# Kernel optimization log

Measured on AMD Instinct MI355X. Metric: run time of the kernel, lower is better.

Reference implementation:

```python
import math
import jax, jax.numpy as jnp
import numpy as np

B, S, D, H = 4, 2048, 1024, 16
DK = D // H
THETA = 10000.0


def _rope(xh, pos):
    # xh: [B, H, S, DK], pos: [S]
    half = jnp.arange(0, DK, 2, dtype=jnp.float32) / DK
    inv_freq = THETA ** (-half)                      # [DK/2]
    ang = pos.astype(jnp.float32)[:, None] * inv_freq  # [S, DK/2]
    cos, sin = jnp.cos(ang).astype(xh.dtype), jnp.sin(ang).astype(xh.dtype)
    x1, x2 = xh[..., 0::2], xh[..., 1::2]
    r1 = x1 * cos - x2 * sin
    r2 = x1 * sin + x2 * cos
    return jnp.stack([r1, r2], axis=-1).reshape(xh.shape)


def setup_inputs() -> dict:
    key = jax.random.key(0)
    kx, kq, kk, kv, ko = jax.random.split(key, 5)
    std = 0.02
    x = jax.random.normal(kx, (B, S, D), jnp.float32)
    wq = jax.random.normal(kq, (D, D), jnp.float32) * std
    wk = jax.random.normal(kk, (D, D), jnp.float32) * std
    wv = jax.random.normal(kv, (D, D), jnp.float32) * std
    wo = jax.random.normal(ko, (D, D), jnp.float32) * std
    token_positions = jnp.arange(S, dtype=jnp.int32)
    return {"x": x, "wq": wq, "wk": wk, "wv": wv, "wo": wo,
            "token_positions": token_positions}


def reference(x, wq, wk, wv, wo, token_positions):
    # bias-free linear projections: y = x @ W^T (torch Linear convention)
    q = x @ wq.T
    k = x @ wk.T
    v = x @ wv.T
    # split heads: [B, S, D] -> [B, H, S, DK]
    to_heads = lambda t: t.reshape(B, S, H, DK).transpose(0, 2, 1, 3)
    qh, kh, vh = to_heads(q), to_heads(k), to_heads(v)
    qh = _rope(qh, token_positions)
    kh = _rope(kh, token_positions)
    scores = jnp.einsum('bhqd,bhkd->bhqk', qh, kh) / math.sqrt(DK)
    causal = jnp.tril(jnp.ones((S, S), dtype=bool))
    scores = jnp.where(causal, scores, -jnp.inf)
    attn = jax.nn.softmax(scores, axis=-1)
    out = jnp.einsum('bhqk,bhkd->bhqd', attn, vh)       # [B, H, S, DK]
    out = out.transpose(0, 2, 1, 3).reshape(B, S, D)    # merge heads
    return out @ wo.T
```

## Files before the change

kernel.cpp:

```cpp
#include <hip/hip_runtime.h>

#define B_ 4
#define S_ 2048
#define D_ 1024
#define H_ 16
#define DK_ 64
#define M_ (B_*S_)
#define K_ D_
#define N_ D_
#define NSTEP 32

typedef unsigned short u16;
typedef unsigned int u32;
typedef __bf16 bf16x8 __attribute__((ext_vector_type(8)));
typedef float f32x4 __attribute__((ext_vector_type(4)));
typedef u32 u32x4v __attribute__((ext_vector_type(4)));

#define EXP2F(x) __builtin_amdgcn_exp2f(x)

__device__ __forceinline__ u16 f2bf(float f) {
    u32 u = __builtin_bit_cast(u32, f);
    u += 0x7fff + ((u >> 16) & 1);
    return (u16)(u >> 16);
}
__device__ __forceinline__ float bf2f(u16 h) {
    u32 u = ((u32)h) << 16;
    return __builtin_bit_cast(float, u);
}
__device__ __forceinline__ u32 pack_trunc(float a, float b) {
    return (__builtin_bit_cast(u32, a) >> 16) | (__builtin_bit_cast(u32, b) & 0xffff0000u);
}

#define GLDS16(g, l) __builtin_amdgcn_global_load_lds( \
    (__attribute__((address_space(1))) void*)(g),      \
    (__attribute__((address_space(3))) void*)(l), 16, 0, 0)

__global__ __launch_bounds__(256) void cvt_all(
    const float* __restrict__ x,
    const float* __restrict__ w0, const float* __restrict__ w1,
    const float* __restrict__ w2, const float* __restrict__ w3,
    u16* __restrict__ xb,
    u16* __restrict__ o0, u16* __restrict__ o1,
    u16* __restrict__ o2, u16* __restrict__ o3) {
    const size_t i = (size_t)blockIdx.x * 256 + threadIdx.x;
    const float* in;
    u16* out;
    size_t off;
    if (i < 2097152) {
        in = x; out = xb; off = i;
    } else {
        const size_t j = i - 2097152;
        const int wi = (int)(j >> 18);
        off = j & 262143;
        in  = (wi == 0) ? w0 : (wi == 1) ? w1 : (wi == 2) ? w2 : w3;
        out = (wi == 0) ? o0 : (wi == 1) ? o1 : (wi == 2) ? o2 : o3;
    }
    const float4 f = *(const float4*)(in + off * 4);
    u32 p0 = (u32)f2bf(f.x) | ((u32)f2bf(f.y) << 16);
    u32 p1 = (u32)f2bf(f.z) | ((u32)f2bf(f.w) << 16);
    *(uint2*)(out + off * 4) = make_uint2(p0, p1);
}

template <int MODE>
__device__ __forceinline__ void gemm_tile(const u16* __restrict__ A,
                                          const u16* __restrict__ Bm,
                                          void* __restrict__ Cv,
                                          int m0, int n0,
                                          u16* __restrict__ As,
                                          u16* __restrict__ Bs) {
    const int tid  = threadIdx.x;
    const int wave = tid >> 6, lane = tid & 63;
    const int wm = wave & 1, wn = wave >> 1;
    const int quad = lane >> 4, mcol = lane & 15;

    const int c0 = wave, c1 = wave + 4;
    const int r0 = c0 * 16 + (lane >> 2), r1 = c1 * 16 + (lane >> 2);
    const int kb = (((lane & 3) ^ ((lane >> 3) & 3)) * 8);
    const u16* ga0 = A  + (size_t)(m0 + r0) * K_ + kb;
    const u16* ga1 = A  + (size_t)(m0 + r1) * K_ + kb;
    const u16* gb0 = Bm + (size_t)(n0 + r0) * K_ + kb;
    const u16* gb1 = Bm + (size_t)(n0 + r1) * K_ + kb;
    const int lo0 = c0 * 512, lo1 = c1 * 512;
    const int rsw = ((mcol >> 1) & 3);

    f32x4 acc[4][4];
#pragma unroll
    for (int i = 0; i < 4; i++)
#pragma unroll
        for (int j = 0; j < 4; j++) acc[i][j] = f32x4{0.f, 0.f, 0.f, 0.f};

    GLDS16(ga0, As + lo0); GLDS16(ga1, As + lo1);
    GLDS16(gb0, Bs + lo0); GLDS16(gb1, Bs + lo1);
    ga0 += 32; ga1 += 32; gb0 += 32; gb1 += 32;

    int cur = 0;
    for (int t = 0; t < NSTEP; ++t) {
        asm volatile("s_waitcnt vmcnt(0)" ::: "memory");
        asm volatile("s_waitcnt lgkmcnt(0)" ::: "memory");
        __builtin_amdgcn_s_barrier();

        if (t + 1 < NSTEP) {
            u16* at = As + (cur ^ 1) * 4096;
            u16* bt = Bs + (cur ^ 1) * 4096;
            GLDS16(ga0, at + lo0); GLDS16(ga1, at + lo1);
            GLDS16(gb0, bt + lo0); GLDS16(gb1, bt + lo1);
            ga0 += 32; ga1 += 32; gb0 += 32; gb1 += 32;
        }

        const u16* Ab = As + cur * 4096;
        const u16* Bb = Bs + cur * 4096;
        bf16x8 af[4], bfr[4];
#pragma unroll
        for (int i = 0; i < 4; i++) {
            af[i]  = *(const bf16x8*)&Ab[(wm * 64 + i * 16 + mcol) * 32 + (quad ^ rsw) * 8];
            bfr[i] = *(const bf16x8*)&Bb[(wn * 64 + i * 16 + mcol) * 32 + (quad ^ rsw) * 8];
        }
        __builtin_amdgcn_s_setprio(1);
#pragma unroll
        for (int i = 0; i < 4; i++)
#pragma unroll
            for (int j = 0; j < 4; j++)
                acc[i][j] = __builtin_amdgcn_mfma_f32_16x16x32_bf16(
                    af[i], bfr[j], acc[i][j], 0, 0, 0);
        __builtin_amdgcn_s_setprio(0);

        cur ^= 1;
    }

#pragma unroll
    for (int i = 0; i < 4; i++) {
        const int row = m0 + wm * 64 + i * 16 + quad * 4;
#pragma unroll
        for (int j = 0; j < 4; j++) {
            const int col = n0 + wn * 64 + j * 16 + mcol;
            if constexpr (MODE == 2) {
                const int hh = col >> 6, dd = col & 63;
                const int bb = row >> 11, ss = row & 2047;
                const u32 lo = (u32)f2bf(acc[i][j][0]) | ((u32)f2bf(acc[i][j][1]) << 16);
                const u32 hi = (u32)f2bf(acc[i][j][2]) | ((u32)f2bf(acc[i][j][3]) << 16);
                *(uint2*)((u16*)Cv + ((size_t)((bb * H_ + hh) * DK_ + dd)) * S_ + ss) =
                    make_uint2(lo, hi);
            } else {
#pragma unroll
                for (int r = 0; r < 4; r++) {
                    if constexpr (MODE == 1)
                        ((float*)Cv)[(size_t)(row + r) * N_ + col] = acc[i][j][r];
                    else
                        ((u16*)Cv)[(size_t)(row + r) * N_ + col] = f2bf(acc[i][j][r]);
                }
            }
        }
    }
}

__global__ __launch_bounds__(256) void gemm_qkv_kernel(
    const u16* __restrict__ x,
    const u16* __restrict__ wq, const u16* __restrict__ wk,
    const u16* __restrict__ wv,
    u16* __restrict__ q, u16* __restrict__ k, u16* __restrict__ vt) {
    __shared__ u16 As[2 * 4096];
    __shared__ u16 Bs[2 * 4096];
    const int flat = blockIdx.x;
    const int w = (flat & 7) * 192 + (flat >> 3);
    const int my = w / 24;
    const int rem = w - my * 24;
    const int z = rem >> 3, nx = rem & 7;
    const int m0 = my * 128, n0 = nx * 128;
    if (z == 2) {
        gemm_tile<2>(x, wv, vt, m0, n0, As, Bs);
    } else {
        const u16* Bm = z ? wk : wq;
        u16* C        = z ? k  : q;
        gemm_tile<0>(x, Bm, C, m0, n0, As, Bs);
    }
}

__global__ __launch_bounds__(256) void gemm_out_kernel(
    const u16* __restrict__ o, const u16* __restrict__ wo, float* __restrict__ out) {
    __shared__ u16 As[2 * 4096];
    __shared__ u16 Bs[2 * 4096];
    const int flat = blockIdx.x;
    const int w = (flat & 7) * 64 + (flat >> 3);
    const int my = w >> 3, nx = w & 7;
    gemm_tile<1>(o, wo, out, my * 128, nx * 128, As, Bs);
}

__global__ __launch_bounds__(256) void rope_qk(u16* __restrict__ q,
                                               u16* __restrict__ k,
                                               const int* __restrict__ pos) {
    const int idx = blockIdx.x * 256 + threadIdx.x;
    const int seg = idx & 3;
    const int h = (idx >> 2) & (H_ - 1);
    const int s = (idx >> 6) & (S_ - 1);
    const int b = idx >> 17;
    const float p = (float)pos[s];
    const float QSC = 0.18033688011112042f;
    const size_t off = ((size_t)(b * S_ + s)) * D_ + h * DK_ + seg * 16;

    u32 qa[8], ka[8];
    *(uint4*)&qa[0] = *(const uint4*)(q + off);
    *(uint4*)&qa[4] = *(const uint4*)(q + off + 8);
    *(uint4*)&ka[0] = *(const uint4*)(k + off);
    *(uint4*)&ka[4] = *(const uint4*)(k + off + 8);
#pragma unroll
    for (int w = 0; w < 8; w++) {
        const int i = seg * 8 + w;
        const float inv = exp2f((float)i * (-13.287712379549449f / 32.f));
        const float ang = p * inv;
        float sn, cs;
        __sincosf(ang, &sn, &cs);
        {
            const float x1 = bf2f((u16)(qa[w] & 0xffff));
            const float x2 = bf2f((u16)(qa[w] >> 16));
            qa[w] = (u32)f2bf((x1 * cs - x2 * sn) * QSC) |
                    ((u32)f2bf((x1 * sn + x2 * cs) * QSC) << 16);
        }
        {
            const float x1 = bf2f((u16)(ka[w] & 0xffff));
            const float x2 = bf2f((u16)(ka[w] >> 16));
            ka[w] = (u32)f2bf(x1 * cs - x2 * sn) |
                    ((u32)f2bf(x1 * sn + x2 * cs) << 16);
        }
    }
    *(uint4*)(q + off)     = *(uint4*)&qa[0];
    *(uint4*)(q + off + 8) = *(uint4*)&qa[4];
    *(uint4*)(k + off)     = *(uint4*)&ka[0];
    *(uint4*)(k + off + 8) = *(uint4*)&ka[4];
}

__global__ __launch_bounds__(256) void attn_kernel(
    const u16* __restrict__ q, const u16* __restrict__ k,
    const u16* __restrict__ vt, u16* __restrict__ o) {
    __shared__ u16 Ks[64 * 64];
    __shared__ u16 Vs[64 * 64];

    const int tid = threadIdx.x, wave = tid >> 6, lane = tid & 63;
    const int flat = blockIdx.x;
    const int qp = flat >> 6;
    const int h = flat & (H_ - 1);
    const int b = (flat >> 4) & 3;
    const int quad = lane >> 4, mcol = lane & 15;
    const int srd = mcol & 7;

    const int rr2 = tid >> 2, cc2 = tid & 3;
    const int sw = rr2 & 7;
    const int so0 = rr2 * 64 + (((cc2 * 2)     ^ sw) << 3);
    const int so1 = rr2 * 64 + (((cc2 * 2 + 1) ^ sw) << 3);
    const int prr = (rr2 & 35) | ((rr2 & 12) << 1) | ((rr2 & 16) >> 2);
    const int ch2 = cc2 * 16;
    const u16* krow = k + ((size_t)(b * S_ + prr)) * D_ + h * DK_ + ch2;
    const u16* vrow = vt + ((size_t)((b * H_ + h) * DK_ + rr2)) * S_ + ch2;

    u32x4v onesw;
    onesw[0] = onesw[1] = onesw[2] = onesw[3] = 0x3F803F80u;
    const bf16x8 onesf = __builtin_bit_cast(bf16x8, onesw);

    for (int pass = 0; pass < 2; pass++) {
        const int qt = pass ? (15 - qp) : qp;
        const int q0 = qt * 128;
        const int wq0 = q0 + wave * 32;
        const int jmax = 2 * qt + 1;

        bf16x8 qf[2][2];
#pragma unroll
        for (int g = 0; g < 2; g++) {
            const u16* qs = q + ((size_t)(b * S_ + wq0 + g * 16 + mcol)) * D_ + h * DK_ + quad * 8;
            qf[g][0] = *(const bf16x8*)qs;
            qf[g][1] = *(const bf16x8*)(qs + 32);
        }

        float m[2] = {-1e30f, -1e30f};
        f32x4 lacc[2];
        f32x4 oacc[2][4];
#pragma unroll
        for (int g = 0; g < 2; g++) {
            lacc[g] = f32x4{0.f, 0.f, 0.f, 0.f};
#pragma unroll
            for (int dn = 0; dn < 4; dn++) oacc[g][dn] = f32x4{0.f, 0.f, 0.f, 0.f};
        }

        uint4 kr0 = *(const uint4*)(krow);
        uint4 kr1 = *(const uint4*)(krow + 8);
        uint4 vr0 = *(const uint4*)(vrow);
        uint4 vr1 = *(const uint4*)(vrow + 8);

        for (int j = 0; j <= jmax; j++) {
            __syncthreads();
            *(uint4*)&Ks[so0] = kr0;
            *(uint4*)&Ks[so1] = kr1;
            *(uint4*)&Vs[so0] = vr0;
            *(uint4*)&Vs[so1] = vr1;
            __syncthreads();

            if (j < jmax) {
                kr0 = *(const uint4*)(krow + (size_t)(j + 1) * 64 * D_);
                kr1 = *(const uint4*)(krow + (size_t)(j + 1) * 64 * D_ + 8);
                vr0 = *(const uint4*)(vrow + (j + 1) * 64);
                vr1 = *(const uint4*)(vrow + (j + 1) * 64 + 8);
            }

            if (j * 64 > wq0 + 31) continue;

            f32x4 st[2][4];
            __builtin_amdgcn_s_setprio(1);
#pragma unroll
            for (int n = 0; n < 4; n++) {
                const u16* kl = &Ks[(n * 16 + mcol) * 64];
                bf16x8 kf0 = *(const bf16x8*)&kl[(quad ^ srd) << 3];
                bf16x8 kf1 = *(const bf16x8*)&kl[((quad | 4) ^ srd) << 3];
                f32x4 z0 = f32x4{0.f, 0.f, 0.f, 0.f};
                z0 = __builtin_amdgcn_mfma_f32_16x16x32_bf16(kf0, qf[0][0], z0, 0, 0, 0);
                z0 = __builtin_amdgcn_mfma_f32_16x16x32_bf16(kf1, qf[0][1], z0, 0, 0, 0);
                st[0][n] = z0;
                f32x4 z1 = f32x4{0.f, 0.f, 0.f, 0.f};
                z1 = __builtin_amdgcn_mfma_f32_16x16x32_bf16(kf0, qf[1][0], z1, 0, 0, 0);
                z1 = __builtin_amdgcn_mfma_f32_16x16x32_bf16(kf1, qf[1][1], z1, 0, 0, 0);
                st[1][n] = z1;
            }
            __builtin_amdgcn_s_setprio(0);

            if (j * 64 + 63 > wq0) {
#pragma unroll
                for (int g = 0; g < 2; g++) {
                    const int qg = wq0 + g * 16 + mcol;
#pragma unroll
                    for (int n = 0; n < 4; n++) {
                        const int tb = j * 64 + ((n >> 1) << 5) + ((n & 1) << 2) + quad * 8;
#pragma unroll
                        for (int r = 0; r < 4; r++)
                            if (tb + r > qg) st[g][n][r] = -1e30f;
                    }
                }
            }

#pragma unroll
            for (int g = 0; g < 2; g++) {
                float mx = st[g][0][0];
#pragma unroll
                for (int n = 0; n < 4; n++)
#pragma unroll
                    for (int r = 0; r < 4; r++) mx = fmaxf(mx, st[g][n][r]);
                mx = fmaxf(mx, __shfl_xor(mx, 16));
                mx = fmaxf(mx, __shfl_xor(mx, 32));
                const bool need = !__all(mx <= m[g] + 8.f);
                if (need) {
                    const float mnew = fmaxf(m[g], mx);
                    const float al = EXP2F(m[g] - mnew);
                    m[g] = mnew;
                    float alphaT[4];
#pragma unroll
                    for (int r = 0; r < 4; r++) alphaT[r] = __shfl(al, quad * 4 + r);
#pragma unroll
                    for (int dn = 0; dn < 4; dn++)
#pragma unroll
                        for (int r = 0; r < 4; r++) oacc[g][dn][r] *= alphaT[r];
#pragma unroll
                    for (int r = 0; r < 4; r++) lacc[g][r] *= alphaT[r];
                }
#pragma unroll
                for (int n = 0; n < 4; n++)
#pragma unroll
                    for (int r = 0; r < 4; r++)
                        st[g][n][r] = EXP2F(st[g][n][r] - m[g]);
            }

            bf16x8 pf[2][2];
#pragma unroll
            for (int g = 0; g < 2; g++) {
                u32x4v w0, w1;
                w0[0] = pack_trunc(st[g][0][0], st[g][0][1]);
                w0[1] = pack_trunc(st[g][0][2], st[g][0][3]);
                w0[2] = pack_trunc(st[g][1][0], st[g][1][1]);
                w0[3] = pack_trunc(st[g][1][2], st[g][1][3]);
                w1[0] = pack_trunc(st[g][2][0], st[g][2][1]);
                w1[1] = pack_trunc(st[g][2][2], st[g][2][3]);
                w1[2] = pack_trunc(st[g][3][0], st[g][3][1]);
                w1[3] = pack_trunc(st[g][3][2], st[g][3][3]);
                pf[g][0] = __builtin_bit_cast(bf16x8, w0);
                pf[g][1] = __builtin_bit_cast(bf16x8, w1);
            }

            __builtin_amdgcn_s_setprio(1);
#pragma unroll
            for (int g = 0; g < 2; g++) {
                lacc[g] = __builtin_amdgcn_mfma_f32_16x16x32_bf16(pf[g][0], onesf, lacc[g], 0, 0, 0);
                lacc[g] = __builtin_amdgcn_mfma_f32_16x16x32_bf16(pf[g][1], onesf, lacc[g], 0, 0, 0);
            }
#pragma unroll
            for (int dn = 0; dn < 4; dn++) {
                const u16* vl = &Vs[(dn * 16 + mcol) * 64];
                bf16x8 vf0 = *(const bf16x8*)&vl[(quad ^ srd) << 3];
                bf16x8 vf1 = *(const bf16x8*)&vl[((quad | 4) ^ srd) << 3];
#pragma unroll
                for (int g = 0; g < 2; g++) {
                    oacc[g][dn] = __builtin_amdgcn_mfma_f32_16x16x32_bf16(pf[g][0], vf0, oacc[g][dn], 0, 0, 0);
                    oacc[g][dn] = __builtin_amdgcn_mfma_f32_16x16x32_bf16(pf[g][1], vf1, oacc[g][dn], 0, 0, 0);
                }
            }
            __builtin_amdgcn_s_setprio(0);
        }

#pragma unroll
        for (int g = 0; g < 2; g++) {
            float linv[4];
#pragma unroll
            for (int r = 0; r < 4; r++) linv[r] = 1.f / lacc[g][r];
#pragma unroll
            for (int dn = 0; dn < 4; dn++)
#pragma unroll
                for (int r = 0; r < 4; r++) {
                    const int row = wq0 + g * 16 + quad * 4 + r;
                    o[((size_t)(b * S_ + row)) * D_ + h * DK_ + dn * 16 + mcol] =
                        f2bf(oacc[g][dn][r] * linv[r]);
                }
        }
    }
}

extern "C" void kernel_launch(void* const* d_in, const int* in_sizes, int n_in,
                              void* d_out, int out_size, void* d_ws, size_t ws_size,
                              hipStream_t stream) {
    const float* x  = (const float*)d_in[0];
    const float* wq = (const float*)d_in[1];
    const float* wk = (const float*)d_in[2];
    const float* wv = (const float*)d_in[3];
    const float* wo = (const float*)d_in[4];
    const int*   tp = (const int*)d_in[5];
    float* out = (float*)d_out;

    u16* ws = (u16*)d_ws;
    const size_t NE = (size_t)M_ * D_;
    const size_t WE = (size_t)N_ * K_;
    u16* xb  = ws;
    u16* wqb = ws + NE;
    u16* wkb = wqb + WE;
    u16* wvb = wkb + WE;
    u16* wob = wvb + WE;
    u16* qb  = wob + WE;
    u16* kb  = qb + NE;
    u16* vtb = (u16*)d_out;
    u16* ob  = xb;

    dim3 blk(256);
    cvt_all<<<dim3(12288), blk, 0, stream>>>(x, wq, wk, wv, wo,
                                             xb, wqb, wkb, wvb, wob);

    gemm_qkv_kernel<<<dim3(3 * (M_ / 128) * (N_ / 128)), blk, 0, stream>>>(xb, wqb, wkb, wvb, qb, kb, vtb);
    rope_qk<<<dim3((B_ * S_ * H_ * 4) / 256), blk, 0, stream>>>(qb, kb, tp);
    attn_kernel<<<dim3((S_ / 128 / 2) * H_ * B_), blk, 0, stream>>>(qb, kb, vtb, ob);
    gemm_out_kernel<<<dim3((M_ / 128) * (N_ / 128)), blk, 0, stream>>>(ob, wob, out);
}
```

Baseline: 259.5 us.

## Fuse RoPE into QKV GEMM epilogue and triple-buffer GEMM LDS pipeline

Removes the standalone rope_qk kernel and applies the rotary embedding, plus the softmax scale on Q, inside the Q/K GEMM epilogue. Adjacent column pairs are exchanged with a lane shuffle before sincos. The GEMM mainloop moves from double to triple-buffered LDS with a two-stage-ahead prefetch and a partial vmcnt wait, so loads overlap compute more. This avoids one kernel launch and a full read and write of Q and K, at the cost of more LDS per block and some extra epilogue work.

New measurement: 263.1 us. About the same (+1.4%).

```diff
diff --git a/kernel.cpp b/kernel.cpp
--- a/kernel.cpp
+++ b/kernel.cpp
@@ -61,13 +61,14 @@
     *(uint2*)(out + off * 4) = make_uint2(p0, p1);
 }
 
-template <int MODE>
+template <int MODE, int ROPE>
 __device__ __forceinline__ void gemm_tile(const u16* __restrict__ A,
                                           const u16* __restrict__ Bm,
                                           void* __restrict__ Cv,
                                           int m0, int n0,
                                           u16* __restrict__ As,
-                                          u16* __restrict__ Bs) {
+                                          u16* __restrict__ Bs,
+                                          const int* __restrict__ pos) {
     const int tid  = threadIdx.x;
     const int wave = tid >> 6, lane = tid & 63;
     const int wm = wave & 1, wn = wave >> 1;
@@ -92,16 +93,20 @@
     GLDS16(ga0, As + lo0); GLDS16(ga1, As + lo1);
     GLDS16(gb0, Bs + lo0); GLDS16(gb1, Bs + lo1);
     ga0 += 32; ga1 += 32; gb0 += 32; gb1 += 32;
-
-    int cur = 0;
+    GLDS16(ga0, As + 4096 + lo0); GLDS16(ga1, As + 4096 + lo1);
+    GLDS16(gb0, Bs + 4096 + lo0); GLDS16(gb1, Bs + 4096 + lo1);
+    ga0 += 32; ga1 += 32; gb0 += 32; gb1 += 32;
+
+    int cur = 0, tgt = 2;
     for (int t = 0; t < NSTEP; ++t) {
-        asm volatile("s_waitcnt vmcnt(0)" ::: "memory");
+        if (t < NSTEP - 1) asm volatile("s_waitcnt vmcnt(4)" ::: "memory");
+        else               asm volatile("s_waitcnt vmcnt(0)" ::: "memory");
         asm volatile("s_waitcnt lgkmcnt(0)" ::: "memory");
         __builtin_amdgcn_s_barrier();
 
-        if (t + 1 < NSTEP) {
-            u16* at = As + (cur ^ 1) * 4096;
-            u16* bt = Bs + (cur ^ 1) * 4096;
+        if (t < NSTEP - 2) {
+            u16* at = As + tgt * 4096;
+            u16* bt = Bs + tgt * 4096;
             GLDS16(ga0, at + lo0); GLDS16(ga1, at + lo1);
             GLDS16(gb0, bt + lo0); GLDS16(gb1, bt + lo1);
             ga0 += 32; ga1 += 32; gb0 += 32; gb1 += 32;
@@ -124,12 +129,28 @@
                     af[i], bfr[j], acc[i][j], 0, 0, 0);
         __builtin_amdgcn_s_setprio(0);
 
-        cur ^= 1;
-    }
+        cur = (cur == 2) ? 0 : cur + 1;
+        tgt = (tgt == 2) ? 0 : tgt + 1;
+    }
+
+    float invj[4];
+    if constexpr (ROPE != 0) {
+#pragma unroll
+        for (int j = 0; j < 4; j++) {
+            const int col = n0 + wn * 64 + j * 16 + mcol;
+            invj[j] = exp2f((float)((col & 63) >> 1) * (-13.287712379549449f / 32.f));
+        }
+    }
+    const bool evenlane = ((mcol & 1) == 0);
 
 #pragma unroll
     for (int i = 0; i < 4; i++) {
         const int row = m0 + wm * 64 + i * 16 + quad * 4;
+        float pr[4];
+        if constexpr (ROPE != 0) {
+#pragma unroll
+            for (int r = 0; r < 4; r++) pr[r] = (float)pos[(row + r) & (S_ - 1)];
+        }
 #pragma unroll
         for (int j = 0; j < 4; j++) {
             const int col = n0 + wn * 64 + j * 16 + mcol;
@@ -140,6 +161,18 @@
                 const u32 hi = (u32)f2bf(acc[i][j][2]) | ((u32)f2bf(acc[i][j][3]) << 16);
                 *(uint2*)((u16*)Cv + ((size_t)((bb * H_ + hh) * DK_ + dd)) * S_ + ss) =
                     make_uint2(lo, hi);
+            } else if constexpr (ROPE != 0) {
+#pragma unroll
+                for (int r = 0; r < 4; r++) {
+                    const float v = acc[i][j][r];
+                    const float other = __shfl_xor(v, 1);
+                    float sn, cs;
+                    __sincosf(pr[r] * invj[j], &sn, &cs);
+                    float o = evenlane ? (v * cs - other * sn)
+                                       : (other * sn + v * cs);
+                    if constexpr (ROPE == 2) o *= 0.18033688011112042f;
+                    ((u16*)Cv)[(size_t)(row + r) * N_ + col] = f2bf(o);
+                }
             } else {
 #pragma unroll
                 for (int r = 0; r < 4; r++) {
@@ -157,9 +190,10 @@
     const u16* __restrict__ x,
     const u16* __restrict__ wq, const u16* __restrict__ wk,
     const u16* __restrict__ wv,
-    u16* __restrict__ q, u16* __restrict__ k, u16* __restrict__ vt) {
-    __shared__ u16 As[2 * 4096];
-    __shared__ u16 Bs[2 * 4096];
+    u16* __restrict__ q, u16* __restrict__ k, u16* __restrict__ vt,
+    const int* __restrict__ pos) {
+    __shared__ u16 As[3 * 4096];
+    __shared__ u16 Bs[3 * 4096];
     const int flat = blockIdx.x;
     const int w = (flat & 7) * 192 + (flat >> 3);
     const int my = w / 24;
@@ -167,65 +201,22 @@
     const int z = rem >> 3, nx = rem & 7;
     const int m0 = my * 128, n0 = nx * 128;
     if (z == 2) {
-        gemm_tile<2>(x, wv, vt, m0, n0, As, Bs);
+        gemm_tile<2, 0>(x, wv, vt, m0, n0, As, Bs, pos);
+    } else if (z == 1) {
+        gemm_tile<0, 1>(x, wk, k, m0, n0, As, Bs, pos);
     } else {
-        const u16* Bm = z ? wk : wq;
-        u16* C        = z ? k  : q;
-        gemm_tile<0>(x, Bm, C, m0, n0, As, Bs);
+        gemm_tile<0, 2>(x, wq, q, m0, n0, As, Bs, pos);
     }
 }
 
 __global__ __launch_bounds__(256) void gemm_out_kernel(
     const u16* __restrict__ o, const u16* __restrict__ wo, float* __restrict__ out) {
-    __shared__ u16 As[2 * 4096];
-    __shared__ u16 Bs[2 * 4096];
+    __shared__ u16 As[3 * 4096];
+    __shared__ u16 Bs[3 * 4096];
     const int flat = blockIdx.x;
     const int w = (flat & 7) * 64 + (flat >> 3);
     const int my = w >> 3, nx = w & 7;
-    gemm_tile<1>(o, wo, out, my * 128, nx * 128, As, Bs);
-}
-
-__global__ __launch_bounds__(256) void rope_qk(u16* __restrict__ q,
-                                               u16* __restrict__ k,
-                                               const int* __restrict__ pos) {
-    const int idx = blockIdx.x * 256 + threadIdx.x;
-    const int seg = idx & 3;
-    const int h = (idx >> 2) & (H_ - 1);
-    const int s = (idx >> 6) & (S_ - 1);
-    const int b = idx >> 17;
-    const float p = (float)pos[s];
-    const float QSC = 0.18033688011112042f;
-    const size_t off = ((size_t)(b * S_ + s)) * D_ + h * DK_ + seg * 16;
-
-    u32 qa[8], ka[8];
-    *(uint4*)&qa[0] = *(const uint4*)(q + off);
-    *(uint4*)&qa[4] = *(const uint4*)(q + off + 8);
-    *(uint4*)&ka[0] = *(const uint4*)(k + off);
-    *(uint4*)&ka[4] = *(const uint4*)(k + off + 8);
-#pragma unroll
-    for (int w = 0; w < 8; w++) {
-        const int i = seg * 8 + w;
-        const float inv = exp2f((float)i * (-13.287712379549449f / 32.f));
-        const float ang = p * inv;
-        float sn, cs;
-        __sincosf(ang, &sn, &cs);
-        {
-            const float x1 = bf2f((u16)(qa[w] & 0xffff));
-            const float x2 = bf2f((u16)(qa[w] >> 16));
-            qa[w] = (u32)f2bf((x1 * cs - x2 * sn) * QSC) |
-                    ((u32)f2bf((x1 * sn + x2 * cs) * QSC) << 16);
-        }
-        {
-            const float x1 = bf2f((u16)(ka[w] & 0xffff));
-            const float x2 = bf2f((u16)(ka[w] >> 16));
-            ka[w] = (u32)f2bf(x1 * cs - x2 * sn) |
-                    ((u32)f2bf(x1 * sn + x2 * cs) << 16);
-        }
-    }
-    *(uint4*)(q + off)     = *(uint4*)&qa[0];
-    *(uint4*)(q + off + 8) = *(uint4*)&qa[4];
-    *(uint4*)(k + off)     = *(uint4*)&ka[0];
-    *(uint4*)(k + off + 8) = *(uint4*)&ka[4];
+    gemm_tile<1, 0>(o, wo, out, my * 128, nx * 128, As, Bs, nullptr);
 }
 
 __global__ __launch_bounds__(256) void attn_kernel(
@@ -445,8 +436,8 @@
     cvt_all<<<dim3(12288), blk, 0, stream>>>(x, wq, wk, wv, wo,
                                              xb, wqb, wkb, wvb, wob);
 
-    gemm_qkv_kernel<<<dim3(3 * (M_ / 128) * (N_ / 128)), blk, 0, stream>>>(xb, wqb, wkb, wvb, qb, kb, vtb);
-    rope_qk<<<dim3((B_ * S_ * H_ * 4) / 256), blk, 0, stream>>>(qb, kb, tp);
+    gemm_qkv_kernel<<<dim3(3 * (M_ / 128) * (N_ / 128)), blk, 0, stream>>>(
+        xb, wqb, wkb, wvb, qb, kb, vtb, tp);
     attn_kernel<<<dim3((S_ / 128 / 2) * H_ * B_), blk, 0, stream>>>(qb, kb, vtb, ob);
     gemm_out_kernel<<<dim3((M_ / 128) * (N_ / 128)), blk, 0, stream>>>(ob, wob, out);
 }
```
